# Optimization experiments

Measured on AMD Instinct MI355X. Metric: run time of the kernel, lower is better.

Reference implementation:

```python
import jax, jax.numpy as jnp
import numpy as np

N = 128            # number of delay lines
BUFFER_LEN = 48000 # delay buffer length (samples)
SCALE = 1.0
N_BINS = 64        # reflection filter taps


def setup_inputs() -> dict:
    key = jax.random.key(0)
    k1, k2, k3, k4 = jax.random.split(key, 4)
    return {
        "buffer": jax.random.normal(k1, (N, BUFFER_LEN), dtype=jnp.float32),
        "inputs": jax.random.normal(k2, (N,), dtype=jnp.float32),
        # fractional delays in samples, in [0, 32)
        "delays": jax.random.uniform(k3, (N,), dtype=jnp.float32) * 32.0,
        "reflection_filters": jax.random.normal(k4, (N, N_BINS), dtype=jnp.float32),
    }


def reference(buffer, inputs, delays, reflection_filters):
    K = 2 * BUFFER_LEN
    # FIFO push: roll left, write newest sample at the end
    buf = jnp.roll(buffer, -1, axis=-1).at[:, -1].set(inputs)
    # zero-pad to FFT length K
    buffer_pad = jnp.pad(buf, ((0, 0), (0, K - BUFFER_LEN)))
    fft_buffer = jnp.fft.fft(buffer_pad, axis=-1)  # [N, K] complex

    d = SCALE * delays[:, None]  # [N, 1]
    two_pi_over_K = 2.0 * jnp.pi / K
    omega_left = two_pi_over_K * jnp.arange(K // 2, dtype=jnp.float32)[None, :]          # [1, K/2]
    omega_right = two_pi_over_K * (K - jnp.arange(K // 2 + 1, K, dtype=jnp.float32))[None, :]  # [1, K/2-1]

    # Pei-Lai closed-form fractional delay filter
    H_left = jnp.exp(-1j * (omega_left * d))                 # [N, K/2]
    H_mid = jnp.cos(jnp.pi * d).astype(jnp.complex64)        # [N, 1] (Nyquist bin)
    H_right = jnp.exp(1j * (omega_right * d))                # [N, K/2-1]
    H = jnp.concatenate([H_left, H_mid, H_right], axis=1)    # [N, K]

    delayed = jnp.fft.ifft(H * fft_buffer, axis=-1).real.astype(jnp.float32)  # [N, K]

    # weighted slice of the n_bins taps preceding the read head
    taps = delayed[:, BUFFER_LEN - N_BINS - 1 : BUFFER_LEN - 1]  # [N, n_bins]
    outputs = (reflection_filters * taps).sum(-1)                # [N]
    return outputs[:, None]                                      # [N, 1]
```

## Files before the change

### kernel.cpp

```cpp
#include <hip/hip_runtime.h>
#include <hip/hip_bf16.h>
#include <math.h>

#define NLINES 128
#define BUFLEN 48000
#define KLEN   96000
#define NBINS  64
#define TAP1   47936
#define PSLOW  47840
#define NG8    5980
#define G1     3072
#define NREST  860
#define NTHR   1024
#define NW     16
#define NTK    10

#define INV2K  5.2083333333333333e-06f
#define DLT_F  3.2724923474893679e-05f
#define T05    1.6362461737446e-05f
#define T15    4.9087385252705e-05f
#define T25    8.1812308687e-05f
#define T35    1.1453723216e-04f

__device__ __forceinline__ float wave_reduce(float v){
  #pragma unroll
  for (int off = 32; off; off >>= 1) v += __shfl_down(v, off, 64);
  return v;
}

__device__ __forceinline__ float sin_pi_d(float d){
  const float r = rintf(d);
  float sp = __builtin_amdgcn_sinf(0.5f * (d - r));
  if (((int)r) & 1) sp = -sp;
  return sp;
}

__global__ __launch_bounds__(NTHR) void frac_delay_part(
    const float* __restrict__ buffer, const float* __restrict__ inputs,
    const float* __restrict__ delays, const float* __restrict__ filt,
    float* __restrict__ ws)
{
  const int line = blockIdx.x >> 1;
  const int role = blockIdx.x & 1;
  const int tid  = threadIdx.x;
  const int lane = tid & 63, wv = tid >> 6;

  __shared__ float redM[NW][5];
  __shared__ float redT[NW][NBINS];

  const float d = delays[line];
  const float scale0 = sin_pi_d(d) * (1.0f / (float)KLEN);
  const float* __restrict__ bufline = buffer + (size_t)line * BUFLEN;

  const float cb = 47964.0f - d;
  float A0=0.f, A1=0.f, A2=0.f, A3=0.f, A4=0.f;

  auto moment8 = [&](int P, float4 va, float4 vb){
    const float tr = (cb - (float)P) * INV2K;
    const float s  = __builtin_amdgcn_sinf(tr);
    const float c  = __builtin_amdgcn_cosf(tr);
    const float TBL[8] = {T35, T25, T15, T05, -T05, -T15, -T25, -T35};
    const float vv[8]  = {va.x, va.y, va.z, va.w, vb.x, vb.y, vb.z, vb.w};
    float N[8], D[8], Pp[8], w[8];
    #pragma unroll
    for (int i = 0; i < 8; ++i){
      N[i] = fmaf(s, -TBL[i], c);
      D[i] = fmaf(c,  TBL[i], s);
    }
    Pp[0] = D[0];
    #pragma unroll
    for (int i = 1; i < 8; ++i) Pp[i] = Pp[i-1] * D[i];
    float inv = __builtin_amdgcn_rcpf(Pp[7]);
    #pragma unroll
    for (int i = 7; i >= 1; --i){ w[i] = N[i] * (inv * Pp[i-1]); inv *= D[i]; }
    w[0] = N[0] * inv;
    #pragma unroll
    for (int i = 0; i < 8; ++i){
      const float vp = (i & 1) ? -vv[i] : vv[i];
      const float W  = w[i];
      const float w2 = W * W;
      const float u  = w2 + 1.0f;
      A0 = fmaf(vp, W, A0);
      const float vu = vp * u;
      A1 += vu;
      const float t2 = vu * W;
      A2 += t2;
      const float e3 = fmaf(3.0f, w2, 1.0f);
      A3 = fmaf(vu, e3, A3);
      A4 = fmaf(t2, e3 + 1.0f, A4);
    }
  };

  if (role == 0){
    int P = tid << 3;
    float4 va = *reinterpret_cast<const float4*>(bufline + P);
    float4 vb = *reinterpret_cast<const float4*>(bufline + P + 4);
    if (tid == 0) va.x = 0.f;
    #pragma unroll
    for (int k = 0; k < 3; ++k){
      int Pn = 0; float4 na, nb;
      if (k < 2){
        Pn = (tid + (k + 1) * NTHR) << 3;
        na = *reinterpret_cast<const float4*>(bufline + Pn);
        nb = *reinterpret_cast<const float4*>(bufline + Pn + 4);
      }
      moment8(P, va, vb);
      P = Pn; va = na; vb = nb;
    }
  } else {
    int P = (G1 + tid) << 3;
    float4 va = *reinterpret_cast<const float4*>(bufline + P);
    float4 vb = *reinterpret_cast<const float4*>(bufline + P + 4);
    #pragma unroll
    for (int k = 0; k < 2; ++k){
      int Pn = 0; float4 na, nb;
      const bool more = (k < 1) || (tid < NREST);
      if (more){
        Pn = (G1 + (k + 1) * NTHR + tid) << 3;
        na = *reinterpret_cast<const float4*>(bufline + Pn);
        nb = *reinterpret_cast<const float4*>(bufline + Pn + 4);
      }
      moment8(P, va, vb);
      P = Pn; va = na; vb = nb;
    }
    if (tid < NREST) moment8(P, va, vb);
  }

  float tj = 0.f;
  if (role == 1){
    const int j  = lane;
    const int jj = TAP1 + j;
    #pragma unroll
    for (int k = 0; k < NTK; ++k){
      const int p = PSLOW + wv + (k << 4);
      const float v = bufline[p];
      const float x = (float)(jj - p) - d;
      float term;
      if (x == 0.0f) term = v;
      else {
        const float tr = x * INV2K;
        const float ct = __builtin_amdgcn_cosf(tr) *
                         __builtin_amdgcn_rcpf(__builtin_amdgcn_sinf(tr));
        const float sg = ((j + p) & 1) ? 1.0f : -1.0f;
        term = sg * scale0 * v * ct;
      }
      tj += term;
    }
    if (wv == 0){
      const float v = inputs[line];
      const int   p = BUFLEN;
      const float x = (float)(jj - p) - d;
      const float tr = x * INV2K;
      const float ct = __builtin_amdgcn_cosf(tr) *
                       __builtin_amdgcn_rcpf(__builtin_amdgcn_sinf(tr));
      const float sg = ((j + p) & 1) ? 1.0f : -1.0f;
      tj += sg * scale0 * v * ct;
    }
  }

  float vals[5] = {A0, A1, A2, A3, A4};
  #pragma unroll
  for (int k = 0; k < 5; ++k){
    float x = wave_reduce(vals[k]);
    if (lane == 0) redM[wv][k] = x;
  }
  redT[wv][lane] = tj;
  __syncthreads();

  if (wv == 0){
    float mom[5];
    #pragma unroll
    for (int k = 0; k < 5; ++k){
      float s = 0.f;
      #pragma unroll
      for (int w = 0; w < NW; ++w) s += redM[w][k];
      mom[k] = s;
    }
    float tail = 0.f;
    if (role == 1){
      #pragma unroll
      for (int w = 0; w < NW; ++w) tail += redT[w][lane];
    }
    const float Y = ((float)lane - 31.5f) * DLT_F;
    float h =          mom[4] * (1.0f/3.0f);
    h = fmaf(h, Y,    -mom[3] * (1.0f/3.0f));
    h = fmaf(h, Y,     mom[2]);
    h = fmaf(h, Y,    -mom[1]);
    h = fmaf(h, Y,     mom[0]);
    const float sg = (lane & 1) ? 1.0f : -1.0f;
    const float tap = fmaf(sg * scale0, h, tail);
    float val = tap * filt[line * NBINS + lane];
    val = wave_reduce(val);
    if (lane == 0) ws[blockIdx.x] = val;
  }
}

__global__ __launch_bounds__(NLINES) void frac_delay_combine(
    const float* __restrict__ ws, float* __restrict__ out)
{
  const int t = threadIdx.x;
  out[t] = ws[2 * t] + ws[2 * t + 1];
}

extern "C" void kernel_launch(void* const* d_in, const int* in_sizes, int n_in,
                              void* d_out, int out_size, void* d_ws, size_t ws_size,
                              hipStream_t stream)
{
  const float* buffer = (const float*)d_in[0];
  const float* inputs = (const float*)d_in[1];
  const float* delays = (const float*)d_in[2];
  const float* filt   = (const float*)d_in[3];
  float* out = (float*)d_out;
  float* ws  = (float*)d_ws;

  frac_delay_part<<<2 * NLINES, NTHR, 0, stream>>>(buffer, inputs, delays, filt, ws);
  frac_delay_combine<<<1, NLINES, 0, stream>>>(ws, out);
}
```

Measured before the change: 14.21 us.

## Fuse combine step into main kernel via flag-based cross-block handoff

Drops the second combine kernel. The role-1 block of each line now publishes its partial sum together with a magic flag as one packed 64-bit atomic store. The role-0 block spin-waits on that flag, then writes the final output itself. The moment-sum work is also rebalanced: role 0 takes more 8-sample groups, and role 1 takes fewer groups plus the tail taps. The risks are that the flag in the workspace is never cleared between calls, so a later call can read a stale partial, and that the spin-wait depends on both blocks of a line being co-resident.

```diff
diff --git a/kernel.cpp b/kernel.cpp
--- a/kernel.cpp
+++ b/kernel.cpp
@@ -9,11 +9,12 @@
 #define TAP1   47936
 #define PSLOW  47840
 #define NG8    5980
-#define G1     3072
-#define NREST  860
+#define G0END  4352
+#define R1REST 604
 #define NTHR   1024
 #define NW     16
 #define NTK    10
+#define FLAGV  0x5A17F00Du
 
 #define INV2K  5.2083333333333333e-06f
 #define DLT_F  3.2724923474893679e-05f
@@ -38,7 +39,7 @@
 __global__ __launch_bounds__(NTHR) void frac_delay_part(
     const float* __restrict__ buffer, const float* __restrict__ inputs,
     const float* __restrict__ delays, const float* __restrict__ filt,
-    float* __restrict__ ws)
+    unsigned long long* __restrict__ ws, float* __restrict__ out)
 {
   const int line = blockIdx.x >> 1;
   const int role = blockIdx.x & 1;
@@ -91,43 +92,38 @@
     }
   };
 
+  float tj = 0.f;
   if (role == 0){
     int P = tid << 3;
     float4 va = *reinterpret_cast<const float4*>(bufline + P);
     float4 vb = *reinterpret_cast<const float4*>(bufline + P + 4);
     if (tid == 0) va.x = 0.f;
     #pragma unroll
-    for (int k = 0; k < 3; ++k){
+    for (int k = 0; k < 4; ++k){
       int Pn = 0; float4 na, nb;
-      if (k < 2){
-        Pn = (tid + (k + 1) * NTHR) << 3;
+      const bool more = (k < 3) || (tid < 256);
+      if (more){
+        Pn = (k < 3) ? ((tid + (k + 1) * NTHR) << 3) : ((4096 + tid) << 3);
         na = *reinterpret_cast<const float4*>(bufline + Pn);
         nb = *reinterpret_cast<const float4*>(bufline + Pn + 4);
       }
       moment8(P, va, vb);
       P = Pn; va = na; vb = nb;
     }
+    if (tid < 256) moment8(P, va, vb);
   } else {
-    int P = (G1 + tid) << 3;
+    int P = (G0END + tid) << 3;
     float4 va = *reinterpret_cast<const float4*>(bufline + P);
     float4 vb = *reinterpret_cast<const float4*>(bufline + P + 4);
-    #pragma unroll
-    for (int k = 0; k < 2; ++k){
-      int Pn = 0; float4 na, nb;
-      const bool more = (k < 1) || (tid < NREST);
-      if (more){
-        Pn = (G1 + (k + 1) * NTHR + tid) << 3;
-        na = *reinterpret_cast<const float4*>(bufline + Pn);
-        nb = *reinterpret_cast<const float4*>(bufline + Pn + 4);
-      }
-      moment8(P, va, vb);
-      P = Pn; va = na; vb = nb;
-    }
-    if (tid < NREST) moment8(P, va, vb);
-  }
-
-  float tj = 0.f;
-  if (role == 1){
+    int Pn = 0; float4 na, nb;
+    if (tid < R1REST){
+      Pn = (G0END + NTHR + tid) << 3;
+      na = *reinterpret_cast<const float4*>(bufline + Pn);
+      nb = *reinterpret_cast<const float4*>(bufline + Pn + 4);
+    }
+    moment8(P, va, vb);
+    if (tid < R1REST) moment8(Pn, na, nb);
+
     const int j  = lane;
     const int jj = TAP1 + j;
     #pragma unroll
@@ -191,15 +187,20 @@
     const float tap = fmaf(sg * scale0, h, tail);
     float val = tap * filt[line * NBINS + lane];
     val = wave_reduce(val);
-    if (lane == 0) ws[blockIdx.x] = val;
+    if (lane == 0){
+      if (role == 1){
+        const unsigned long long pk =
+            ((unsigned long long)FLAGV << 32) | (unsigned long long)__float_as_uint(val);
+        __hip_atomic_store(&ws[line], pk, __ATOMIC_RELEASE, __HIP_MEMORY_SCOPE_AGENT);
+      } else {
+        unsigned long long pk;
+        do {
+          pk = __hip_atomic_load(&ws[line], __ATOMIC_ACQUIRE, __HIP_MEMORY_SCOPE_AGENT);
+        } while ((unsigned)(pk >> 32) != FLAGV);
+        out[line] = val + __uint_as_float((unsigned)pk);
+      }
+    }
   }
-}
-
-__global__ __launch_bounds__(NLINES) void frac_delay_combine(
-    const float* __restrict__ ws, float* __restrict__ out)
-{
-  const int t = threadIdx.x;
-  out[t] = ws[2 * t] + ws[2 * t + 1];
 }
 
 extern "C" void kernel_launch(void* const* d_in, const int* in_sizes, int n_in,
@@ -211,8 +212,7 @@
   const float* delays = (const float*)d_in[2];
   const float* filt   = (const float*)d_in[3];
   float* out = (float*)d_out;
-  float* ws  = (float*)d_ws;
-
-  frac_delay_part<<<2 * NLINES, NTHR, 0, stream>>>(buffer, inputs, delays, filt, ws);
-  frac_delay_combine<<<1, NLINES, 0, stream>>>(ws, out);
-}
+  unsigned long long* ws = (unsigned long long*)d_ws;
+
+  frac_delay_part<<<2 * NLINES, NTHR, 0, stream>>>(buffer, inputs, delays, filt, ws, out);
+}
```

Measured after the change: 14.50 us. 1.02x slower.
